# Performance work log

Hardware: AMD Instinct MI355X
Metric: run time of the kernel (lower is better)

## Reference

```python
import jax, jax.numpy as jnp
import numpy as np

UP = 2      # up_ratio
K = 3       # kernel_size
EPS = 1e-5  # BatchNorm eps


def _bn(x, g, b, m, v):
    # eval-mode BatchNorm2d over channel axis 1 of NCHW
    scale = g / jnp.sqrt(v + EPS)
    return x * scale[:, None, None] + (b - m * scale)[:, None, None]


def setup_inputs() -> dict:
    key = jax.random.key(0)
    ks = jax.random.split(key, 13)
    N, C, H, W = 8, 256, 64, 64
    OC = 64
    P = UP * UP * K * K  # 36 encoder output channels
    return {
        "x": jax.random.normal(ks[0], (N, C, H, W), jnp.float32),
        "w0": jax.random.normal(ks[1], (OC, C), jnp.float32) * 0.05,
        "b0": jax.random.normal(ks[2], (OC,), jnp.float32) * 0.05,
        "bn0_g": jax.random.uniform(ks[3], (OC,), jnp.float32, 0.5, 1.5),
        "bn0_b": jax.random.normal(ks[4], (OC,), jnp.float32) * 0.05,
        "bn0_m": jax.random.normal(ks[5], (OC,), jnp.float32) * 0.05,
        "bn0_v": jax.random.uniform(ks[6], (OC,), jnp.float32, 0.5, 1.5),
        "w1": jax.random.normal(ks[7], (P, OC), jnp.float32) * 0.05,
        "b1": jax.random.normal(ks[8], (P,), jnp.float32) * 0.05,
        "bn1_g": jax.random.uniform(ks[9], (P,), jnp.float32, 0.5, 1.5),
        "bn1_b": jax.random.normal(ks[10], (P,), jnp.float32) * 0.05,
        "bn1_m": jax.random.normal(ks[11], (P,), jnp.float32) * 0.05,
        "bn1_v": jax.random.uniform(ks[12], (P,), jnp.float32, 0.5, 1.5),
    }


def reference(x, w0, b0, bn0_g, bn0_b, bn0_m, bn0_v,
              w1, b1, bn1_g, bn1_b, bn1_m, bn1_v):
    N, C, H, W = x.shape
    k2, u2 = K * K, UP * UP

    # layer0: 1x1 conv + BN + ReLU
    y = jnp.einsum('nchw,oc->nohw', x, w0) + b0[:, None, None]
    y = jax.nn.relu(_bn(y, bn0_g, bn0_b, bn0_m, bn0_v))

    # encoder: 1x1 conv + BN + ReLU -> (N, u2*k2, H, W)
    enc = jnp.einsum('nohw,po->nphw', y, w1) + b1[:, None, None]
    enc = jax.nn.relu(_bn(enc, bn1_g, bn1_b, bn1_m, bn1_v))

    # pixelshuffle(UP) + softmax over k2 + unfold back to low-res is
    # algebraically: split channels as (k2, u2) and softmax over k2.
    # channel index = k*u2 + r*UP + s, matching torch PixelShuffle layout.
    wts = jax.nn.softmax(enc.reshape(N, k2, u2, H, W), axis=1)  # n k u h w

    # im2col on input: ZeroPad2d(1) + 3x3 unfold -> (N, C, k2, H, W)
    pad = K // 2
    xp = jnp.pad(x, ((0, 0), (0, 0), (pad, pad), (pad, pad)))
    patches = jnp.stack([xp[:, :, i:i + H, j:j + W]
                         for i in range(K) for j in range(K)], axis=2)

    out = jnp.einsum('nckhw,nkuhw->ncuhw', patches, wts)  # (N, C, u2, H, W)

    # pixelshuffle: u = r*UP + s places value at (h*UP+r, w*UP+s)
    out = out.reshape(N, C, UP, UP, H, W)
    out = out.transpose(0, 1, 4, 2, 5, 3).reshape(N, C, H * UP, W * UP)
    return out
```

## Files before the change

kernel.cpp:

```cpp
#include <hip/hip_runtime.h>


#define EPS_BN 1e-5f

typedef float f32x4 __attribute__((ext_vector_type(4)));

__global__ __launch_bounds__(256) void carafe_encoder(
    const float* __restrict__ x,
    const float* __restrict__ w0, const float* __restrict__ b0,
    const float* __restrict__ g0, const float* __restrict__ be0,
    const float* __restrict__ m0, const float* __restrict__ v0,
    const float* __restrict__ w1, const float* __restrict__ b1,
    const float* __restrict__ g1, const float* __restrict__ be1,
    const float* __restrict__ m1, const float* __restrict__ v1,
    float* __restrict__ wts)
{
    __shared__ float xs[256 * 64];
    __shared__ float ys[64 * 64];

    const int tid = threadIdx.x;
    const int n   = blockIdx.x >> 6;
    const int hh  = blockIdx.x & 63;
    const int w   = tid & 63;
    const int og  = __builtin_amdgcn_readfirstlane(tid >> 6);

    {
        const f32x4* xg = reinterpret_cast<const f32x4*>(x + (n * 256) * 4096 + hh * 64);
        f32x4* xl = reinterpret_cast<f32x4*>(xs);
#pragma unroll
        for (int k = 0; k < 16; ++k) {
            const int i  = tid + k * 256;
            const int cc = i >> 4;
            const int c4 = i & 15;
            xl[cc * 16 + c4] = xg[cc * 1024 + c4];
        }
    }
    __syncthreads();

    float acc[16];
#pragma unroll
    for (int j = 0; j < 16; ++j) acc[j] = 0.f;

    const float* w0p = w0 + og * 16 * 256;

#pragma unroll 8
    for (int c = 0; c < 256; ++c) {
        const float xv = xs[c * 64 + w];
#pragma unroll
        for (int j = 0; j < 16; ++j)
            acc[j] = fmaf(xv, w0p[j * 256 + c], acc[j]);
    }

#pragma unroll
    for (int j = 0; j < 16; ++j) {
        const int o = og * 16 + j;
        const float sc = g0[o] * rsqrtf(v0[o] + EPS_BN);
        const float sh = (b0[o] - m0[o]) * sc + be0[o];
        ys[o * 64 + w] = fmaxf(fmaf(acc[j], sc, sh), 0.f);
    }
    __syncthreads();

    float e9[9];
#pragma unroll
    for (int kk = 0; kk < 9; ++kk) e9[kk] = 0.f;
    const int u = og;
    const float* w1p = w1 + u * 64;
#pragma unroll 4
    for (int o = 0; o < 64; ++o) {
        const float yv = ys[o * 64 + w];
#pragma unroll
        for (int kk = 0; kk < 9; ++kk)
            e9[kk] = fmaf(yv, w1p[kk * 256 + o], e9[kk]);
    }

    float mx = -1e30f;
#pragma unroll
    for (int kk = 0; kk < 9; ++kk) {
        const int p = kk * 4 + u;
        const float sc = g1[p] * rsqrtf(v1[p] + EPS_BN);
        const float sh = (b1[p] - m1[p]) * sc + be1[p];
        float e = fmaxf(fmaf(e9[kk], sc, sh), 0.f);
        e9[kk] = e;
        mx = fmaxf(mx, e);
    }
    float s = 0.f;
#pragma unroll
    for (int kk = 0; kk < 9; ++kk) {
        e9[kk] = __expf(e9[kk] - mx);
        s += e9[kk];
    }
    const float inv = 1.f / s;
#pragma unroll
    for (int kk = 0; kk < 9; ++kk)
        wts[((n * 36 + kk * 4 + u) * 64 + hh) * 64 + w] = e9[kk] * inv;
}

__global__ __launch_bounds__(256) void carafe_reassemble(
    const float* __restrict__ x,
    const float* __restrict__ wts,
    float* __restrict__ out)
{
    const int t  = blockIdx.x * 256 + threadIdx.x;
    const int w  = t & 63;
    const int h  = (t >> 6) & 63;
    const int cg = (t >> 12) & 63;
    const int n  = t >> 18;

    float wt[36];
    const float* wp = wts + (n * 36) * 4096 + h * 64 + w;
#pragma unroll
    for (int p = 0; p < 36; ++p) wt[p] = wp[p * 4096];

#pragma unroll
    for (int i = 0; i < 4; ++i) {
        const int c = cg * 4 + i;
        const float* xp = x + (n * 256 + c) * 4096;
        float a0 = 0.f, a1 = 0.f, a2 = 0.f, a3 = 0.f;
#pragma unroll
        for (int dh = -1; dh <= 1; ++dh) {
            const int hhp = h + dh;
            const bool hv = (hhp >= 0) & (hhp < 64);
#pragma unroll
            for (int dw = -1; dw <= 1; ++dw) {
                const int wwp = w + dw;
                const bool vv = hv & (wwp >= 0) & (wwp < 64);
                const float xv = vv ? xp[hhp * 64 + wwp] : 0.f;
                const int k = (dh + 1) * 3 + (dw + 1);
                a0 = fmaf(xv, wt[k * 4 + 0], a0);
                a1 = fmaf(xv, wt[k * 4 + 1], a1);
                a2 = fmaf(xv, wt[k * 4 + 2], a2);
                a3 = fmaf(xv, wt[k * 4 + 3], a3);
            }
        }
        float* op = out + ((n * 256 + c) * 128 + 2 * h) * 128 + 2 * w;
        float2 r0; r0.x = a0; r0.y = a1;
        float2 r1; r1.x = a2; r1.y = a3;
        *reinterpret_cast<float2*>(op)       = r0;
        *reinterpret_cast<float2*>(op + 128) = r1;
    }
}

extern "C" void kernel_launch(void* const* d_in, const int* in_sizes, int n_in,
                              void* d_out, int out_size, void* d_ws, size_t ws_size,
                              hipStream_t stream)
{
    const float* x   = (const float*)d_in[0];
    const float* w0  = (const float*)d_in[1];
    const float* b0  = (const float*)d_in[2];
    const float* g0  = (const float*)d_in[3];
    const float* be0 = (const float*)d_in[4];
    const float* m0  = (const float*)d_in[5];
    const float* v0  = (const float*)d_in[6];
    const float* w1  = (const float*)d_in[7];
    const float* b1  = (const float*)d_in[8];
    const float* g1  = (const float*)d_in[9];
    const float* be1 = (const float*)d_in[10];
    const float* m1  = (const float*)d_in[11];
    const float* v1  = (const float*)d_in[12];

    float* wts = (float*)d_ws;
    float* out = (float*)d_out;

    hipLaunchKernelGGL(carafe_encoder, dim3(512), dim3(256), 0, stream,
                       x, w0, b0, g0, be0, m0, v0, w1, b1, g1, be1, m1, v1, wts);
    hipLaunchKernelGGL(carafe_reassemble, dim3(8192), dim3(256), 0, stream,
                       x, wts, out);
}
```

Measured before the change: 238.6 us.

## Fuse encoder and reassembly into one kernel reusing shared-memory input row

Merges the encoder and reassembly kernels into a single launch per (batch, row) block. Softmax weights go to shared memory instead of a global workspace, and the centre input row is read from the already-staged shared tile, so only the neighbouring rows come from global memory. This removes the workspace round trip and one launch. The cost is far less parallelism in reassembly (512 blocks, each thread looping over 64 channels instead of 8192 blocks), and the 80KB shared footprint limits occupancy.

```diff
diff --git a/kernel.cpp b/kernel.cpp
--- a/kernel.cpp
+++ b/kernel.cpp
@@ -5,7 +5,7 @@
 
 typedef float f32x4 __attribute__((ext_vector_type(4)));
 
-__global__ __launch_bounds__(256) void carafe_encoder(
+__global__ __launch_bounds__(256) void carafe_fused(
     const float* __restrict__ x,
     const float* __restrict__ w0, const float* __restrict__ b0,
     const float* __restrict__ g0, const float* __restrict__ be0,
@@ -13,7 +13,7 @@
     const float* __restrict__ w1, const float* __restrict__ b1,
     const float* __restrict__ g1, const float* __restrict__ be1,
     const float* __restrict__ m1, const float* __restrict__ v1,
-    float* __restrict__ wts)
+    float* __restrict__ out)
 {
     __shared__ float xs[256 * 64];
     __shared__ float ys[64 * 64];
@@ -42,7 +42,6 @@
     for (int j = 0; j < 16; ++j) acc[j] = 0.f;
 
     const float* w0p = w0 + og * 16 * 256;
-
 #pragma unroll 8
     for (int c = 0; c < 256; ++c) {
         const float xv = xs[c * 64 + w];
@@ -90,49 +89,59 @@
         s += e9[kk];
     }
     const float inv = 1.f / s;
+
+    __syncthreads();
+    float* ws = ys;
 #pragma unroll
     for (int kk = 0; kk < 9; ++kk)
-        wts[((n * 36 + kk * 4 + u) * 64 + hh) * 64 + w] = e9[kk] * inv;
-}
+        ws[(kk * 4 + u) * 64 + w] = e9[kk] * inv;
+    __syncthreads();
 
-__global__ __launch_bounds__(256) void carafe_reassemble(
-    const float* __restrict__ x,
-    const float* __restrict__ wts,
-    float* __restrict__ out)
-{
-    const int t  = blockIdx.x * 256 + threadIdx.x;
-    const int w  = t & 63;
-    const int h  = (t >> 6) & 63;
-    const int cg = (t >> 12) & 63;
-    const int n  = t >> 18;
+    const int q = og;
+    float wt[36];
+#pragma unroll
+    for (int p = 0; p < 36; ++p) wt[p] = ws[p * 64 + w];
 
-    float wt[36];
-    const float* wp = wts + (n * 36) * 4096 + h * 64 + w;
-#pragma unroll
-    for (int p = 0; p < 36; ++p) wt[p] = wp[p * 4096];
+    const bool hm = (hh > 0), hp = (hh < 63);
+    const bool wm = (w > 0),  wp = (w < 63);
 
-#pragma unroll
-    for (int i = 0; i < 4; ++i) {
-        const int c = cg * 4 + i;
-        const float* xp = x + (n * 256 + c) * 4096;
+    for (int c = 0; c < 64; ++c) {
+        const int cc = q * 64 + c;
+        const float* xgm = x + ((n * 256 + cc) * 64 + (hh - 1)) * 64;
+        const float* xgp = x + ((n * 256 + cc) * 64 + (hh + 1)) * 64;
+        const float* xls = xs + cc * 64;
+
         float a0 = 0.f, a1 = 0.f, a2 = 0.f, a3 = 0.f;
-#pragma unroll
-        for (int dh = -1; dh <= 1; ++dh) {
-            const int hhp = h + dh;
-            const bool hv = (hhp >= 0) & (hhp < 64);
-#pragma unroll
-            for (int dw = -1; dw <= 1; ++dw) {
-                const int wwp = w + dw;
-                const bool vv = hv & (wwp >= 0) & (wwp < 64);
-                const float xv = vv ? xp[hhp * 64 + wwp] : 0.f;
-                const int k = (dh + 1) * 3 + (dw + 1);
-                a0 = fmaf(xv, wt[k * 4 + 0], a0);
-                a1 = fmaf(xv, wt[k * 4 + 1], a1);
-                a2 = fmaf(xv, wt[k * 4 + 2], a2);
-                a3 = fmaf(xv, wt[k * 4 + 3], a3);
-            }
+
+        {
+            const float xv0 = (hm & wm) ? xgm[w - 1] : 0.f;
+            const float xv1 = hm        ? xgm[w]     : 0.f;
+            const float xv2 = (hm & wp) ? xgm[w + 1] : 0.f;
+            a0 = fmaf(xv0, wt[0],  fmaf(xv1, wt[4],  xv2 * wt[8]));
+            a1 = fmaf(xv0, wt[1],  fmaf(xv1, wt[5],  xv2 * wt[9]));
+            a2 = fmaf(xv0, wt[2],  fmaf(xv1, wt[6],  xv2 * wt[10]));
+            a3 = fmaf(xv0, wt[3],  fmaf(xv1, wt[7],  xv2 * wt[11]));
         }
-        float* op = out + ((n * 256 + c) * 128 + 2 * h) * 128 + 2 * w;
+        {
+            const float xv0 = wm ? xls[w - 1] : 0.f;
+            const float xv1 = xls[w];
+            const float xv2 = wp ? xls[w + 1] : 0.f;
+            a0 = fmaf(xv0, wt[12], fmaf(xv1, wt[16], fmaf(xv2, wt[20], a0)));
+            a1 = fmaf(xv0, wt[13], fmaf(xv1, wt[17], fmaf(xv2, wt[21], a1)));
+            a2 = fmaf(xv0, wt[14], fmaf(xv1, wt[18], fmaf(xv2, wt[22], a2)));
+            a3 = fmaf(xv0, wt[15], fmaf(xv1, wt[19], fmaf(xv2, wt[23], a3)));
+        }
+        {
+            const float xv0 = (hp & wm) ? xgp[w - 1] : 0.f;
+            const float xv1 = hp        ? xgp[w]     : 0.f;
+            const float xv2 = (hp & wp) ? xgp[w + 1] : 0.f;
+            a0 = fmaf(xv0, wt[24], fmaf(xv1, wt[28], fmaf(xv2, wt[32], a0)));
+            a1 = fmaf(xv0, wt[25], fmaf(xv1, wt[29], fmaf(xv2, wt[33], a1)));
+            a2 = fmaf(xv0, wt[26], fmaf(xv1, wt[30], fmaf(xv2, wt[34], a2)));
+            a3 = fmaf(xv0, wt[27], fmaf(xv1, wt[31], fmaf(xv2, wt[35], a3)));
+        }
+
+        float* op = out + ((n * 256 + cc) * 128 + 2 * hh) * 128 + 2 * w;
         float2 r0; r0.x = a0; r0.y = a1;
         float2 r1; r1.x = a2; r1.y = a3;
         *reinterpret_cast<float2*>(op)       = r0;
@@ -158,11 +167,8 @@
     const float* m1  = (const float*)d_in[11];
     const float* v1  = (const float*)d_in[12];
 
-    float* wts = (float*)d_ws;
     float* out = (float*)d_out;
 
-    hipLaunchKernelGGL(carafe_encoder, dim3(512), dim3(256), 0, stream,
-                       x, w0, b0, g0, be0, m0, v0, w1, b1, g1, be1, m1, v1, wts);
-    hipLaunchKernelGGL(carafe_reassemble, dim3(8192), dim3(256), 0, stream,
-                       x, wts, out);
+    hipLaunchKernelGGL(carafe_fused, dim3(512), dim3(256), 0, stream,
+                       x, w0, b0, g0, be0, m0, v0, w1, b1, g1, be1, m1, v1, out);
 }
```

Result: slower. 244.7 us (+2.6%).
